# Kernel optimization log

Measured on AMD Instinct MI355X. Metric: run time of the kernel, lower is better.

The kernel has to match this reference:

```python
import jax, jax.numpy as jnp
import numpy as np


def setup_inputs() -> dict:
    key = jax.random.key(0)
    k1, k2 = jax.random.split(key)
    B, T, C = 8, 2048, 1024
    x = jax.random.normal(k1, (B, T, C), dtype=jnp.float32)
    y = jax.random.normal(k2, (B, T, C), dtype=jnp.float32)
    return {"x": x, "y": y}


def reference(x, y):
    # Original: x,y -> permute(0,2,1) to [B, C, T]; einsum 'ijk,ilk->ijl'
    # contracts over time -> [B, C, C] correlation matrix; return -mean.
    corr = jnp.einsum('itj,itl->ijl', x, y)  # [B, C, C]
    return -jnp.mean(corr)
```

## Files before the change

kernel.cpp:

```cpp
#include <hip/hip_runtime.h>

#define N_C    1024
#define DENOM  (8.0 * 1024.0 * 1024.0)

#define THREADS 256
#define BLOCKS  2048
#define WAVES   (BLOCKS * THREADS / 64)

__global__ __launch_bounds__(THREADS)
void corr_partial(const float* __restrict__ x,
                  const float* __restrict__ y,
                  float* __restrict__ partials) {
    const int lane = threadIdx.x & 63;
    const int wave = (blockIdx.x * THREADS + threadIdx.x) >> 6;

    const size_t base = (size_t)(2 * wave) * N_C;
    const float4* x0 = (const float4*)(x + base);
    const float4* y0 = (const float4*)(y + base);
    const float4* x1 = (const float4*)(x + base + N_C);
    const float4* y1 = (const float4*)(y + base + N_C);

    float4 ax = {0,0,0,0}, ay = {0,0,0,0}, bx = {0,0,0,0}, by = {0,0,0,0};
    #pragma unroll
    for (int k = 0; k < 4; ++k) {
        float4 vx0 = x0[lane + 64 * k];
        float4 vy0 = y0[lane + 64 * k];
        float4 vx1 = x1[lane + 64 * k];
        float4 vy1 = y1[lane + 64 * k];
        ax.x += vx0.x; ax.y += vx0.y; ax.z += vx0.z; ax.w += vx0.w;
        ay.x += vy0.x; ay.y += vy0.y; ay.z += vy0.z; ay.w += vy0.w;
        bx.x += vx1.x; bx.y += vx1.y; bx.z += vx1.z; bx.w += vx1.w;
        by.x += vy1.x; by.y += vy1.y; by.z += vy1.z; by.w += vy1.w;
    }
    float sx0 = (ax.x + ax.y) + (ax.z + ax.w);
    float sy0 = (ay.x + ay.y) + (ay.z + ay.w);
    float sx1 = (bx.x + bx.y) + (bx.z + bx.w);
    float sy1 = (by.x + by.y) + (by.z + by.w);

    #pragma unroll
    for (int off = 32; off > 0; off >>= 1) {
        sx0 += __shfl_xor(sx0, off, 64);
        sy0 += __shfl_xor(sy0, off, 64);
        sx1 += __shfl_xor(sx1, off, 64);
        sy1 += __shfl_xor(sy1, off, 64);
    }
    if (lane == 0) partials[wave] = sx0 * sy0 + sx1 * sy1;
}

__global__ __launch_bounds__(1024)
void corr_final_reduce(const float* __restrict__ partials,
                       float* __restrict__ out) {
    __shared__ double sdata[1024];
    double acc = 0.0;
    for (int i = threadIdx.x; i < WAVES; i += 1024) acc += (double)partials[i];
    sdata[threadIdx.x] = acc;
    __syncthreads();
    for (int s = 512; s > 0; s >>= 1) {
        if (threadIdx.x < s) sdata[threadIdx.x] += sdata[threadIdx.x + s];
        __syncthreads();
    }
    if (threadIdx.x == 0) out[0] = (float)(-sdata[0] / DENOM);
}

extern "C" void kernel_launch(void* const* d_in, const int* in_sizes, int n_in,
                              void* d_out, int out_size, void* d_ws, size_t ws_size,
                              hipStream_t stream) {
    const float* x = (const float*)d_in[0];
    const float* y = (const float*)d_in[1];
    float* out = (float*)d_out;
    float* partials = (float*)d_ws;

    corr_partial<<<BLOCKS, THREADS, 0, stream>>>(x, y, partials);
    corr_final_reduce<<<1, 1024, 0, stream>>>(partials, out);
}
```

Before: 28.08 us.

## Fuse final reduction into partial kernel via atomic accumulate and last-block ticket

Replaces the two-kernel partial-then-reduce scheme with one kernel. Each 1024-thread block sums its wave results in shared memory and atomically adds the block total into a double accumulator. A ticket counter lets the last block write the final output. This removes the second launch and the partials round-trip, but adds a memset call and 512 contended double atomics, and changes the block size.

```diff
diff --git a/kernel.cpp b/kernel.cpp
--- a/kernel.cpp
+++ b/kernel.cpp
@@ -3,16 +3,20 @@
 #define N_C    1024
 #define DENOM  (8.0 * 1024.0 * 1024.0)
 
-#define THREADS 256
-#define BLOCKS  2048
-#define WAVES   (BLOCKS * THREADS / 64)
+#define THREADS 1024
+#define BLOCKS  512
+#define WPB     (THREADS / 64)
+#define TOTAL_WAVES (BLOCKS * WPB)
 
 __global__ __launch_bounds__(THREADS)
-void corr_partial(const float* __restrict__ x,
-                  const float* __restrict__ y,
-                  float* __restrict__ partials) {
+void corr_fused(const float* __restrict__ x,
+                const float* __restrict__ y,
+                double* __restrict__ acc,
+                unsigned int* __restrict__ ticket,
+                float* __restrict__ out) {
     const int lane = threadIdx.x & 63;
-    const int wave = (blockIdx.x * THREADS + threadIdx.x) >> 6;
+    const int w    = threadIdx.x >> 6;
+    const int wave = blockIdx.x * WPB + w;
 
     const size_t base = (size_t)(2 * wave) * N_C;
     const float4* x0 = (const float4*)(x + base);
@@ -44,22 +48,24 @@
         sx1 += __shfl_xor(sx1, off, 64);
         sy1 += __shfl_xor(sy1, off, 64);
     }
-    if (lane == 0) partials[wave] = sx0 * sy0 + sx1 * sy1;
-}
 
-__global__ __launch_bounds__(1024)
-void corr_final_reduce(const float* __restrict__ partials,
-                       float* __restrict__ out) {
-    __shared__ double sdata[1024];
-    double acc = 0.0;
-    for (int i = threadIdx.x; i < WAVES; i += 1024) acc += (double)partials[i];
-    sdata[threadIdx.x] = acc;
+    __shared__ double sdata[WPB];
+    if (lane == 0) sdata[w] = (double)sx0 * (double)sy0
+                            + (double)sx1 * (double)sy1;
     __syncthreads();
-    for (int s = 512; s > 0; s >>= 1) {
-        if (threadIdx.x < s) sdata[threadIdx.x] += sdata[threadIdx.x + s];
-        __syncthreads();
+
+    if (threadIdx.x == 0) {
+        double bs = 0.0;
+        #pragma unroll
+        for (int i = 0; i < WPB; ++i) bs += sdata[i];
+        atomicAdd(acc, bs);
+        __threadfence();
+        unsigned int t = atomicAdd(ticket, 1u);
+        if (t == BLOCKS - 1) {
+            double total = atomicAdd(acc, 0.0);
+            out[0] = (float)(-total / DENOM);
+        }
     }
-    if (threadIdx.x == 0) out[0] = (float)(-sdata[0] / DENOM);
 }
 
 extern "C" void kernel_launch(void* const* d_in, const int* in_sizes, int n_in,
@@ -68,8 +74,9 @@
     const float* x = (const float*)d_in[0];
     const float* y = (const float*)d_in[1];
     float* out = (float*)d_out;
-    float* partials = (float*)d_ws;
+    double* acc = (double*)d_ws;
+    unsigned int* ticket = (unsigned int*)((char*)d_ws + 8);
 
-    corr_partial<<<BLOCKS, THREADS, 0, stream>>>(x, y, partials);
-    corr_final_reduce<<<1, 1024, 0, stream>>>(partials, out);
+    hipMemsetAsync(d_ws, 0, 16, stream);
+    corr_fused<<<BLOCKS, THREADS, 0, stream>>>(x, y, acc, ticket, out);
 }
```

After: 44.92 us. 1.6x slower.
